# Kernel optimization log

Measured on AMD Instinct MI355X. Metric: run time of the kernel, lower is better.

The kernel has to match this reference:

```python
import jax, jax.numpy as jnp
import numpy as np

D, P, MC = 512, 256, 128   # state dim, obs dim, control dim
H, M, T = 32, 64, 1024     # num filters, Hankel/filter length, horizon
GAMMA = 0.9


def setup_inputs() -> dict:
    rng = np.random.default_rng(0)
    # Stable dynamics: scale spectral radius to 0.95
    A = rng.standard_normal((D, D)).astype(np.float32)
    A *= np.float32(0.95 / np.max(np.abs(np.linalg.eigvals(A))))
    B = (rng.standard_normal((D, MC)) / np.sqrt(D)).astype(np.float32)
    C = (rng.standard_normal((P, D)) / np.sqrt(D)).astype(np.float32)
    # SPD cost matrices
    Q_obs = np.eye(P, dtype=np.float32)
    R = (0.1 * np.eye(MC)).astype(np.float32)
    # LQR-like feedback gain (small, applied to y_obs as in the source)
    K = (0.02 * rng.standard_normal((MC, P))).astype(np.float32)
    # Spectral filters from Hankel matrix: Z_ij = gamma^(i+j+2) * 2/((i+j+2)^3-(i+j+2))
    idx = np.arange(M)
    ij = idx[:, None] + idx[None, :] + 2
    Z = (GAMMA ** ij) * 2.0 / (ij ** 3 - ij)
    w, V = np.linalg.eigh(Z)
    sigma = np.abs(w[-H:])
    phi = V[:, -H:]
    sigma_phi = (sigma ** 0.25)[:, None] * phi.T        # [H, M]
    sigma_phi_M = sigma_phi.astype(np.float32)
    # sum over the inner l-loop of sigma_phi_m (the source sums contributions over l)
    s_m = sigma_phi.sum(axis=1).astype(np.float32)       # [H]
    # Learned controller tensor M_il -> [m_control, H, h, p]
    M_tensor = (0.01 * rng.standard_normal((MC, H, H, P))).astype(np.float32)
    x0 = rng.standard_normal(D).astype(np.float32)
    return {
        "A": jnp.asarray(A), "B": jnp.asarray(B), "C": jnp.asarray(C),
        "Q_obs": jnp.asarray(Q_obs), "R": jnp.asarray(R), "K": jnp.asarray(K),
        "M_tensor": jnp.asarray(M_tensor),
        "sigma_phi_M": jnp.asarray(sigma_phi_M), "s_m": jnp.asarray(s_m),
        "x0": jnp.asarray(x0),
    }


def reference(A, B, C, Q_obs, R, K, M_tensor, sigma_phi_M, s_m, x0):
    h, m = sigma_phi_M.shape          # filters, history window
    mc = B.shape[1]
    p = C.shape[0]

    # CAB[i] = C @ A^i @ B for i = 0..h  (Markov parameters for y_nat)
    def pow_step(Ap, _):
        return Ap @ A, C @ (Ap @ B)
    _, CAB = jax.lax.scan(pow_step, jnp.eye(A.shape[0], dtype=A.dtype), None, length=h + 1)  # [h+1, p, mc]

    # Pre-contract M_tensor with the inner filter weights (sum over j/l):
    # u_pert[c] = sum_{i,k,p'} M2[c,i,p'] * sigma_phi_M[i,k] * y_nat_{t-k}[p']
    M2 = jnp.einsum('cijq,j->ciq', M_tensor, s_m)  # [mc, h, p]

    def step(carry, _):
        x, u_buf, y_buf = carry            # x:[d], u_buf:[h+1,mc] newest-first, y_buf:[m,p] newest-first
        y_obs = C @ x                      # [p]
        # natural observation: strip effect of past controls
        y_nat = y_obs - jnp.einsum('ipc,ic->p', CAB, u_buf)
        y_buf = jnp.concatenate([y_nat[None, :], y_buf[:-1]], axis=0)
        # spectral projection of y_nat history, then contract with learned tensor
        y_proj = sigma_phi_M @ y_buf       # [h, p]
        u_pert = jnp.einsum('ciq,iq->c', M2, y_proj)  # [mc]
        u = -(K @ y_obs) + u_pert
        cost = y_obs @ (Q_obs @ y_obs) + u @ (R @ u)
        u_buf = jnp.concatenate([u[None, :], u_buf[:-1]], axis=0)
        x = A @ x + B @ u
        return (x, u_buf, y_buf), cost

    init = (x0,
            jnp.zeros((h + 1, mc), dtype=x0.dtype),
            jnp.zeros((m, p), dtype=x0.dtype))
    _, costs = jax.lax.scan(step, init, None, length=T)
    return costs  # [T] per-step losses
```

## Files before the change

kernel.cpp:

```cpp
#include <hip/hip_runtime.h>

#define TPB 256
#define MAXJ 48

#define SC_N 128
#define YD0 128
#define YU0 144
#define WD0 151
#define WU0 159
#define DT0 166
#define XP0 182
#define XR0 214
#define U0 230
#define NWG 238
#define NGRP 8
#define GCH 30

__device__ __forceinline__ void cst(float* p, float v) {
  __hip_atomic_store(p, v, __ATOMIC_RELAXED, __HIP_MEMORY_SCOPE_AGENT);
}
__device__ __forceinline__ void cstu(unsigned* p, unsigned v) {
  __hip_atomic_store(p, v, __ATOMIC_RELAXED, __HIP_MEMORY_SCOPE_AGENT);
}
__device__ __forceinline__ unsigned cldu(const unsigned* p) {
  return __hip_atomic_load(p, __ATOMIC_RELAXED, __HIP_MEMORY_SCOPE_AGENT);
}
__device__ __forceinline__ float cld(const float* p) {
  return __hip_atomic_load(p, __ATOMIC_RELAXED, __HIP_MEMORY_SCOPE_AGENT);
}
__device__ __forceinline__ float2 cld2(const float* p) {
  unsigned long long u = __hip_atomic_load(
      reinterpret_cast<const unsigned long long*>(p), __ATOMIC_RELAXED,
      __HIP_MEMORY_SCOPE_AGENT);
  float2 v;
  __builtin_memcpy(&v, &u, 8);
  return v;
}

__device__ __forceinline__ void grid_barrier(unsigned* __restrict__ arr,
                                             unsigned* __restrict__ grp,
                                             int bid, int tid, unsigned phase) {
  asm volatile("s_waitcnt vmcnt(0)" ::: "memory");
  __syncthreads();
  if (tid == 0) cstu(arr + (bid << 5), phase);
  if (bid < NGRP) {
    const int lo = bid * GCH;
    const int n = (NWG - lo < GCH) ? (NWG - lo) : GCH;
    if (tid < n) {
      while (cldu(arr + ((lo + tid) << 5)) < phase) __builtin_amdgcn_s_sleep(1);
    }
    __syncthreads();
    if (tid == 0) cstu(grp + (bid << 5), phase);
  }
  if (tid < NGRP) {
    while (cldu(grp + (tid << 5)) < phase) __builtin_amdgcn_s_sleep(1);
  }
  __atomic_signal_fence(__ATOMIC_SEQ_CST);
  __syncthreads();
}

__device__ void gemm_tile(const float* __restrict__ X, const float* __restrict__ Y,
                          float* __restrict__ Z, int M, int N, int Kd,
                          int mtile, int ntile) {
  __shared__ float Xs[16][65];
  __shared__ float Ys[16][65];
  const int tx = threadIdx.x & 15;
  const int ty = threadIdx.x >> 4;
  const int mbase = mtile * 64;
  const int nbase = ntile * 64;
  float acc[4][4] = {};
  for (int k0 = 0; k0 < Kd; k0 += 16) {
#pragma unroll
    for (int r = 0; r < 4; ++r) {
      int idx = threadIdx.x + 256 * r;
      int mm = idx >> 4, kk = idx & 15;
      int gm = mbase + mm, gk = k0 + kk;
      Xs[kk][mm] = (gm < M && gk < Kd) ? X[(size_t)gm * Kd + gk] : 0.f;
      int nn = idx & 63, k2 = idx >> 6;
      int gn = nbase + nn, gk2 = k0 + k2;
      Ys[k2][nn] = (gk2 < Kd && gn < N) ? Y[(size_t)gk2 * N + gn] : 0.f;
    }
    __syncthreads();
#pragma unroll
    for (int kk = 0; kk < 16; ++kk) {
      float xv[4], yv[4];
#pragma unroll
      for (int a = 0; a < 4; ++a) xv[a] = Xs[kk][ty * 4 + a];
#pragma unroll
      for (int b = 0; b < 4; ++b) yv[b] = Ys[kk][tx * 4 + b];
#pragma unroll
      for (int a = 0; a < 4; ++a)
#pragma unroll
        for (int b = 0; b < 4; ++b) acc[a][b] += xv[a] * yv[b];
    }
    __syncthreads();
  }
#pragma unroll
  for (int a = 0; a < 4; ++a) {
    int gm = mbase + ty * 4 + a;
    if (gm < M) {
#pragma unroll
      for (int b = 0; b < 4; ++b) {
        int gn = nbase + tx * 4 + b;
        if (gn < N) Z[(size_t)gm * N + gn] = acc[a][b];
      }
    }
  }
}

struct JobBatch {
  int n;
  int start[MAXJ + 1];
  int xsel[MAXJ], xoff[MAXJ], ysel[MAXJ], yoff[MAXJ], zoff[MAXJ];
  int M[MAXJ], N[MAXJ], K[MAXJ];
};

__global__ __launch_bounds__(256) void multi_gemm(JobBatch jb,
    const float* __restrict__ A, const float* __restrict__ Bm,
    const float* __restrict__ C, const float* __restrict__ Km,
    float* __restrict__ ws) {
  int b = blockIdx.x;
  int j = 0;
  while (j < jb.n - 1 && b >= jb.start[j + 1]) ++j;
  int rel = b - jb.start[j];
  const float* bases[5] = {ws, A, Bm, C, Km};
  const float* X = bases[jb.xsel[j]] + jb.xoff[j];
  const float* Y = bases[jb.ysel[j]] + jb.yoff[j];
  float* Z = ws + jb.zoff[j];
  int tn = jb.N[j] >> 6;
  gemm_tile(X, Y, Z, jb.M[j], jb.N[j], jb.K[j], rel / tn, rel % tn);
}

__global__ __launch_bounds__(256) void m2_kernel(const float* __restrict__ MT,
    const float* __restrict__ sm, float* __restrict__ M2g) {
  int idx = blockIdx.x * 256 + threadIdx.x;
  if (idx >= 128 * 32 * 256) return;
  int q = idx & 255;
  int ci = idx >> 8;
  const float* base = MT + (size_t)ci * 32 * 256 + q;
  float acc = 0.f;
#pragma unroll
  for (int j = 0; j < 32; ++j) acc += base[j * 256] * sm[j];
  M2g[idx] = acc;
}

__global__ __launch_bounds__(256) void wfir_kernel(const float* __restrict__ M2g,
    const float* __restrict__ Phi, float* __restrict__ W) {
  int idx = blockIdx.x * 256 + threadIdx.x;
  if (idx >= 64 * 32768) return;
  int j = idx >> 15;
  int cq = idx & 32767;
  int c = cq >> 8;
  int q = cq & 255;
  float acc = 0.f;
#pragma unroll
  for (int i = 0; i < 32; ++i)
    acc = fmaf(Phi[(i << 6) | j], M2g[(size_t)(((c << 5) | i) << 8) | q], acc);
  W[idx] = acc;
}

__global__ __launch_bounds__(256) void axpy_acl(const float* __restrict__ A,
    const float* __restrict__ BKC, float* __restrict__ Acl, float* __restrict__ P1) {
  int i = blockIdx.x * 256 + threadIdx.x;
  if (i < 262144) {
    float v = A[i] - BKC[i];
    Acl[i] = v;
    P1[i] = v;
  }
}

__global__ void init_kernel(const float* __restrict__ x0, float* __restrict__ xh,
    float* __restrict__ eh, float* __restrict__ ynh, float* __restrict__ uh0,
    float* __restrict__ dbnd, unsigned* __restrict__ arr,
    unsigned* __restrict__ grp) {
  int i = blockIdx.x * 256 + threadIdx.x;
  int stride = gridDim.x * 256;
  for (int k = i; k < 524288; k += stride) cst(xh + k, 0.f);
  for (int k = i; k < 139264; k += stride) cst(eh + k, 0.f);
  for (int k = i; k < 262144; k += stride) cst(ynh + k, 0.f);
  for (int k = i; k < 8192; k += stride) cst(uh0 + k, 0.f);
  for (int k = i; k < NWG * 32; k += stride) cstu(arr + k, 0u);
  for (int k = i; k < NGRP * 32; k += stride) cstu(grp + k, 0u);
  if (i < 512) cst(dbnd + i, x0[i]);
}

__global__ __launch_bounds__(TPB, 1) void main_kernel(
    const float* __restrict__ B, const float* __restrict__ C,
    const float* __restrict__ x0, const float* __restrict__ Wfir,
    const float* __restrict__ KC, const float* __restrict__ W0C,
    const float* __restrict__ Pp, const float* __restrict__ CAp,
    const float* __restrict__ W0CAp, const float* __restrict__ Rnp,
    const float* __restrict__ AB33p, const float* __restrict__ CAB33p,
    const float* __restrict__ W0CAB33p, const float* __restrict__ A8k,
    float* __restrict__ xh, float* __restrict__ uh0, float* __restrict__ eh,
    float* __restrict__ ynh, float* __restrict__ dbnd,
    unsigned* __restrict__ arr, unsigned* __restrict__ grp) {
  __shared__ float smA[64 * 256];
  __shared__ float smY[8 * 256];
  __shared__ float smV[512];
  __shared__ float smW[8 * 128];
  __shared__ float smVx[8 * 516];
  __shared__ float redsc[4][16];
  const int bid = blockIdx.x;
  const int tid = threadIdx.x;

  if (bid < SC_N) {
    for (int i = tid; i < 16384; i += TPB) {
      int j = i >> 8;
      smA[i] = (j >= 1) ? Wfir[(size_t)j * 32768 + bid * 256 + (i & 255)] : 0.f;
    }
    __syncthreads();
#pragma unroll 1
    for (int ph = 0; ph <= 130; ++ph) {
      if (ph >= 1 && ph < 129) {
        const int Ty = ph * 8 - 8;
        const int c = bid;
        for (int i2 = tid; i2 < 1024; i2 += TPB) {
          float2 v = cld2(ynh + (size_t)Ty * 256 + 2 * i2);
          smY[2 * i2] = v.x;
          smY[2 * i2 + 1] = v.y;
        }
        __syncthreads();
        const int q = tid;
        float yreg[8];
#pragma unroll
        for (int s = 0; s < 8; ++s) yreg[s] = smY[s * 256 + q];
        const int wv = tid >> 6;
        const int lane = tid & 63;
#pragma unroll
        for (int kt = 0; kt < 5; ++kt) {
          const int r0 = 1 + 16 * kt;
          float wreg[23];
#pragma unroll
          for (int i = 0; i < 23; ++i) {
            const int j = r0 - 7 + i;
            wreg[i] = (j >= 1 && j <= 63) ? smA[j * 256 + q] : 0.f;
          }
          float acc[16];
#pragma unroll
          for (int a = 0; a < 16; ++a) acc[a] = 0.f;
#pragma unroll
          for (int a = 0; a < 16; ++a)
#pragma unroll
            for (int s = 0; s < 8; ++s) acc[a] += wreg[a + 7 - s] * yreg[s];
#pragma unroll
          for (int a = 0; a < 16; ++a) {
            float v = acc[a];
            v += __shfl_xor(v, 32);
            v += __shfl_xor(v, 16);
            v += __shfl_xor(v, 8);
            v += __shfl_xor(v, 4);
            v += __shfl_xor(v, 2);
            v += __shfl_xor(v, 1);
            if (lane == 0) redsc[wv][a] = v;
          }
          __syncthreads();
          if (tid < 16) {
            const int r = r0 + tid;
            if (r <= 70) {
              float sum = redsc[0][tid] + redsc[1][tid] + redsc[2][tid] + redsc[3][tid];
              atomicAdd(&eh[(size_t)(Ty + r) * 128 + bid], sum);
            }
          }
          __syncthreads();
        }
        (void)c;
      }
      grid_barrier(arr, grp, bid, tid, (unsigned)(ph + 1));
    }
  } else if (bid < YU0) {
    const int r = bid - YD0;
    const int s = r >> 1;
    const int half = (r & 1) << 7;
    const int row = half + (tid >> 1);
    const int seg = tid & 1;
    const float* Mrow = (s == 0) ? C : (CAp + (size_t)(s - 1) * 131072);
    const float4* m4 = (const float4*)(Mrow + (size_t)row * 512 + seg * 256);
    float4 cm[64];
#pragma unroll
    for (int it = 0; it < 64; ++it) cm[it] = m4[it];
#pragma unroll 1
    for (int ph = 0; ph <= 130; ++ph) {
      if (ph < 128) {
        const int T = ph * 8;
        {
          float2 v = cld2(dbnd + (size_t)ph * 512 + 2 * tid);
          smV[2 * tid] = v.x;
          smV[2 * tid + 1] = v.y;
        }
        __syncthreads();
        const float4* v4 = (const float4*)(smV + seg * 256);
        float a = 0.f;
#pragma unroll
        for (int it = 0; it < 64; ++it) {
          float4 mm = cm[it], vv = v4[it];
          a += mm.x * vv.x + mm.y * vv.y + mm.z * vv.z + mm.w * vv.w;
        }
        a += __shfl_down(a, 1);
        if (seg == 0) atomicAdd(&ynh[(size_t)(T + s) * 256 + row], a);
      }
      grid_barrier(arr, grp, bid, tid, (unsigned)(ph + 1));
    }
  } else if (bid < WD0) {
    const int m = bid - YU0;
    const int row = tid;
    const float4* m4 = (const float4*)(CAB33p + (size_t)m * 32768 + (size_t)row * 128);
    float4 cm[32];
#pragma unroll
    for (int it = 0; it < 32; ++it) cm[it] = m4[it];
#pragma unroll 1
    for (int ph = 0; ph <= 130; ++ph) {
      if (ph < 128) {
        const int T = ph * 8;
        for (int i2 = tid; i2 < 512; i2 += TPB) {
          float2 v = cld2(uh0 + (size_t)(64 + T - 33) * 128 + 2 * i2);
          smW[2 * i2] = v.x;
          smW[2 * i2 + 1] = v.y;
        }
        __syncthreads();
#pragma unroll
        for (int s = 1; s < 8; ++s) {
          if (s > m) {
            const float4* u4 = (const float4*)(smW + (s - m - 1) * 128);
            float a = 0.f;
#pragma unroll
            for (int it = 0; it < 32; ++it) {
              float4 mm = cm[it], vv = u4[it];
              a += mm.x * vv.x + mm.y * vv.y + mm.z * vv.z + mm.w * vv.w;
            }
            atomicAdd(&ynh[(size_t)(T + s) * 256 + row], a);
          }
        }
      }
      grid_barrier(arr, grp, bid, tid, (unsigned)(ph + 1));
    }
  } else if (bid < WU0) {
    const int s = bid - WD0;
    const int row = tid >> 1;
    const int seg = tid & 1;
    const float* Mrow = (s == 0) ? W0C : (W0CAp + (size_t)(s - 1) * 65536);
    const float4* m4 = (const float4*)(Mrow + (size_t)row * 512 + seg * 256);
    float4 cm[64];
#pragma unroll
    for (int it = 0; it < 64; ++it) cm[it] = m4[it];
#pragma unroll 1
    for (int ph = 0; ph <= 130; ++ph) {
      if (ph < 128) {
        const int T = ph * 8;
        {
          float2 v = cld2(dbnd + (size_t)ph * 512 + 2 * tid);
          smV[2 * tid] = v.x;
          smV[2 * tid + 1] = v.y;
        }
        __syncthreads();
        const float4* v4 = (const float4*)(smV + seg * 256);
        float a = 0.f;
#pragma unroll
        for (int it = 0; it < 64; ++it) {
          float4 mm = cm[it], vv = v4[it];
          a += mm.x * vv.x + mm.y * vv.y + mm.z * vv.z + mm.w * vv.w;
        }
        a += __shfl_down(a, 1);
        if (seg == 0) atomicAdd(&eh[(size_t)(T + s) * 128 + row], a);
      }
      grid_barrier(arr, grp, bid, tid, (unsigned)(ph + 1));
    }
  } else if (bid < DT0) {
    const int m = bid - WU0;
    const int row = tid >> 1;
    const int seg = tid & 1;
    const float4* m4 = (const float4*)(W0CAB33p + (size_t)m * 16384 + (size_t)row * 128 + seg * 64);
    float4 cm[16];
#pragma unroll
    for (int it = 0; it < 16; ++it) cm[it] = m4[it];
#pragma unroll 1
    for (int ph = 0; ph <= 130; ++ph) {
      if (ph < 128) {
        const int T = ph * 8;
        for (int i2 = tid; i2 < 512; i2 += TPB) {
          float2 v = cld2(uh0 + (size_t)(64 + T - 33) * 128 + 2 * i2);
          smW[2 * i2] = v.x;
          smW[2 * i2 + 1] = v.y;
        }
        __syncthreads();
#pragma unroll
        for (int s = 1; s < 8; ++s) {
          if (s > m) {
            const float4* u4 = (const float4*)(smW + (s - m - 1) * 128 + seg * 64);
            float a = 0.f;
#pragma unroll
            for (int it = 0; it < 16; ++it) {
              float4 mm = cm[it], vv = u4[it];
              a += mm.x * vv.x + mm.y * vv.y + mm.z * vv.z + mm.w * vv.w;
            }
            a += __shfl_down(a, 1);
            if (seg == 0) atomicAdd(&eh[(size_t)(T + s) * 128 + row], a);
          }
        }
      }
      grid_barrier(arr, grp, bid, tid, (unsigned)(ph + 1));
    }
  } else if (bid < XP0) {
    const int g = bid - DT0;
    const int row = g * 32 + (tid >> 3);
    const int l8 = tid & 7;
    float4 ca[16], cb[32];
    {
      const float4* m4 = (const float4*)(A8k + (size_t)row * 512);
#pragma unroll
      for (int it = 0; it < 16; ++it) ca[it] = m4[it * 8 + l8];
    }
#pragma unroll
    for (int m = 0; m < 8; ++m) {
      const float4* m4 = (const float4*)(AB33p + (size_t)m * 65536 + (size_t)row * 128);
#pragma unroll
      for (int it = 0; it < 4; ++it) cb[m * 4 + it] = m4[it * 8 + l8];
    }
#pragma unroll 1
    for (int ph = 0; ph <= 130; ++ph) {
      if (ph < 127) {
        const int T = ph * 8;
        {
          float2 v = cld2(dbnd + (size_t)ph * 512 + 2 * tid);
          smV[2 * tid] = v.x;
          smV[2 * tid + 1] = v.y;
        }
        for (int i2 = tid; i2 < 512; i2 += TPB) {
          float2 v = cld2(uh0 + (size_t)(64 + T - 33) * 128 + 2 * i2);
          smW[2 * i2] = v.x;
          smW[2 * i2 + 1] = v.y;
        }
        __syncthreads();
        const float4* v4 = (const float4*)smV;
        float a = 0.f;
#pragma unroll
        for (int it = 0; it < 16; ++it) {
          float4 mm = ca[it], vv = v4[it * 8 + l8];
          a += mm.x * vv.x + mm.y * vv.y + mm.z * vv.z + mm.w * vv.w;
        }
#pragma unroll
        for (int m = 0; m < 8; ++m) {
          const float4* w4 = (const float4*)(smW + (7 - m) * 128);
#pragma unroll
          for (int it = 0; it < 4; ++it) {
            float4 mm = cb[m * 4 + it], vv = w4[it * 8 + l8];
            a += mm.x * vv.x + mm.y * vv.y + mm.z * vv.z + mm.w * vv.w;
          }
        }
        a += __shfl_down(a, 4);
        a += __shfl_down(a, 2);
        a += __shfl_down(a, 1);
        if (l8 == 0) cst(&dbnd[(size_t)(ph + 1) * 512 + row], a);
      }
      grid_barrier(arr, grp, bid, tid, (unsigned)(ph + 1));
    }
  } else if (bid < XR0) {
    const int r = bid - XP0;
    const int s = r >> 2;
    const int qtr = (r & 3) << 7;
    const int row = qtr + (tid >> 1);
    const int seg = tid & 1;
    const float4* mp = (const float4*)(Pp + (size_t)s * 262144 + (size_t)row * 512 + seg * 256);
    float4 cm[64];
#pragma unroll
    for (int it = 0; it < 64; ++it) cm[it] = mp[it];
#pragma unroll 1
    for (int ph = 0; ph <= 130; ++ph) {
      if (ph >= 2 && ph < 130) {
        const int Tq = ph * 8 - 16;
        {
          const float* src = (ph == 2) ? x0 : (xh + (size_t)(Tq - 1) * 512);
          float2 v = cld2(src + 2 * tid);
          smV[2 * tid] = v.x;
          smV[2 * tid + 1] = v.y;
        }
        __syncthreads();
        if (ph == 2) {
          if (s == 0) {
            if (seg == 0) atomicAdd(&xh[(size_t)Tq * 512 + row], smV[row]);
          } else {
            const float4* m4 = (const float4*)(Pp + (size_t)(s - 1) * 262144 +
                                               (size_t)row * 512 + seg * 256);
            const float4* v4 = (const float4*)(smV + seg * 256);
            float a = 0.f;
#pragma unroll
            for (int it = 0; it < 64; ++it) {
              float4 mm = m4[it], vv = v4[it];
              a += mm.x * vv.x + mm.y * vv.y + mm.z * vv.z + mm.w * vv.w;
            }
            a += __shfl_down(a, 1);
            if (seg == 0) atomicAdd(&xh[(size_t)(Tq + s) * 512 + row], a);
          }
        } else {
          const float4* v4 = (const float4*)(smV + seg * 256);
          float a = 0.f;
#pragma unroll
          for (int it = 0; it < 64; ++it) {
            float4 mm = cm[it], vv = v4[it];
            a += mm.x * vv.x + mm.y * vv.y + mm.z * vv.z + mm.w * vv.w;
          }
          a += __shfl_down(a, 1);
          if (seg == 0) atomicAdd(&xh[(size_t)(Tq + s) * 512 + row], a);
        }
      }
      grid_barrier(arr, grp, bid, tid, (unsigned)(ph + 1));
    }
  } else if (bid < U0) {
    const int r = bid - XR0;
    const int i = r >> 1;
    const int half = (r & 1) << 8;
    const int row = half + tid;
    const float* Rrow = (i == 0) ? (B + (size_t)row * 128)
                                 : (Rnp + (size_t)(i - 1) * 65536 + (size_t)row * 128);
    const float4* m4 = (const float4*)Rrow;
    float4 cm[32];
#pragma unroll
    for (int it = 0; it < 32; ++it) cm[it] = m4[it];
#pragma unroll 1
    for (int ph = 0; ph <= 130; ++ph) {
      if (ph >= 2 && ph < 130) {
        const int Tq = ph * 8 - 16;
        for (int i2 = tid; i2 < 512; i2 += TPB) {
          int idx = 2 * i2;
          float2 v;
          if (ph == 2 && idx < 128) {
            v.x = 0.f;
            v.y = 0.f;
          } else {
            v = cld2(eh + (size_t)(Tq - 1) * 128 + idx);
          }
          smW[idx] = v.x;
          smW[idx + 1] = v.y;
        }
        __syncthreads();
#pragma unroll
        for (int s = 0; s < 8; ++s) {
          if (s >= i) {
            const float4* e4 = (const float4*)(smW + (s - i) * 128);
            float a = 0.f;
#pragma unroll
            for (int it = 0; it < 32; ++it) {
              float4 mm = cm[it], vv = e4[it];
              a += mm.x * vv.x + mm.y * vv.y + mm.z * vv.z + mm.w * vv.w;
            }
            atomicAdd(&xh[(size_t)(Tq + s) * 512 + row], a);
          }
        }
      }
      grid_barrier(arr, grp, bid, tid, (unsigned)(ph + 1));
    }
  } else {
    const int g = bid - U0;
    const int o = tid >> 1;
    const int par = tid & 1;
    const int s = o >> 4;
    const int lr = o & 15;
    const int row = g * 16 + lr;
    const float4* m4 = (const float4*)(KC + (size_t)row * 512 + par * 256);
    float4 cm[64];
#pragma unroll
    for (int it = 0; it < 64; ++it) cm[it] = m4[it];
#pragma unroll 1
    for (int ph = 0; ph <= 130; ++ph) {
      if (ph >= 3) {
        const int Tu = ph * 8 - 24;
        for (int i2 = tid; i2 < 2048; i2 += TPB) {
          int idx = 2 * i2;
          int rr = idx >> 9;
          int cc = idx & 511;
          float2 v = cld2(xh + (size_t)(Tu + rr) * 512 + cc);
          smVx[rr * 516 + cc] = v.x;
          smVx[rr * 516 + cc + 1] = v.y;
        }
        __syncthreads();
        const float4* v4 = (const float4*)(smVx + s * 516 + par * 256);
        float a = 0.f;
#pragma unroll
        for (int it = 0; it < 64; ++it) {
          float4 mm = cm[it], vv = v4[it];
          a += mm.x * vv.x + mm.y * vv.y + mm.z * vv.z + mm.w * vv.w;
        }
        a += __shfl_down(a, 1);
        if (par == 0) {
          float u = cld(&eh[(size_t)(Tu + s) * 128 + row]) - a;
          cst(&uh0[(size_t)(64 + Tu + s) * 128 + row], u);
        }
      }
      grid_barrier(arr, grp, bid, tid, (unsigned)(ph + 1));
    }
  }
}

__global__ __launch_bounds__(256) void cost_kernel(const float* __restrict__ C,
    const float* __restrict__ Q, const float* __restrict__ R,
    const float* __restrict__ xh, const float* __restrict__ uh0,
    float* __restrict__ out) {
  __shared__ float xs[512];
  __shared__ float ys[256];
  __shared__ float us[128];
  __shared__ float redw[4];
  const int t = blockIdx.x;
  const int tid = threadIdx.x;
  {
    float2 v = cld2(xh + (size_t)t * 512 + 2 * tid);
    xs[2 * tid] = v.x;
    xs[2 * tid + 1] = v.y;
  }
  if (tid < 64) {
    float2 v = cld2(uh0 + (size_t)(64 + t) * 128 + 2 * tid);
    us[2 * tid] = v.x;
    us[2 * tid + 1] = v.y;
  }
  __syncthreads();
  {
    const float4* m4 = (const float4*)(C + (size_t)tid * 512);
    const float4* v4 = (const float4*)xs;
    float a = 0.f;
    for (int it = 0; it < 128; ++it) {
      float4 mm = m4[it], vv = v4[it];
      a += mm.x * vv.x + mm.y * vv.y + mm.z * vv.z + mm.w * vv.w;
    }
    ys[tid] = a;
  }
  __syncthreads();
  float acc;
  {
    const float* Qr = Q + (size_t)tid * 256;
    float qy = 0.f;
    for (int k = 0; k < 256; ++k) qy = fmaf(Qr[k], ys[k], qy);
    acc = qy * ys[tid];
  }
  if (tid < 128) {
    const float* Rr = R + (size_t)tid * 128;
    float ru = 0.f;
    for (int k = 0; k < 128; ++k) ru = fmaf(Rr[k], us[k], ru);
    acc += ru * us[tid];
  }
  float v = acc;
  v += __shfl_xor(v, 32);
  v += __shfl_xor(v, 16);
  v += __shfl_xor(v, 8);
  v += __shfl_xor(v, 4);
  v += __shfl_xor(v, 2);
  v += __shfl_xor(v, 1);
  if ((tid & 63) == 0) redw[tid >> 6] = v;
  __syncthreads();
  if (tid == 0) out[t] = redw[0] + redw[1] + redw[2] + redw[3];
}

extern "C" void kernel_launch(void* const* d_in, const int* in_sizes, int n_in,
                              void* d_out, int out_size, void* d_ws, size_t ws_size,
                              hipStream_t stream) {
  (void)in_sizes; (void)n_in; (void)out_size; (void)ws_size;
  const float* A = (const float*)d_in[0];
  const float* B = (const float*)d_in[1];
  const float* C = (const float*)d_in[2];
  const float* Q = (const float*)d_in[3];
  const float* R = (const float*)d_in[4];
  const float* Km = (const float*)d_in[5];
  const float* MT = (const float*)d_in[6];
  const float* Phi = (const float*)d_in[7];
  const float* sm = (const float*)d_in[8];
  const float* x0 = (const float*)d_in[9];

  float* ws = (float*)d_ws;
  const int oWfir = 0;
  const int oKC = 2097152;
  const int oW0C = 2162688;
  const int oAcl = 2228224;
  const int oP = 2490368;
  const int oCA = 4587520;
  const int oW0CA = 5505024;
  const int oRn = 5963776;
  const int oApB = 6422528;
  const int oAB33 = 6946816;
  const int oCAB33 = 7471104;
  const int oW0CAB33 = 7700480;
  const int oA2 = 7815168;
  const int oA4 = 8077312;
  const int oA8 = 8339456;
  const int oA16 = 8601600;
  const int oA32 = 8863744;
  const int oM2 = 9125888;
  const int oBKC = oM2;
  const int oxh = 10174464;
  const int ouh0 = 10698752;
  const int oeh = 10838016;
  const int oynh = 10977280;
  const int odbnd = 11239424;
  const int oarr = 11306496;
  const int ogrp = oarr + NWG * 32;

  float* xh = ws + oxh;
  float* uh0 = ws + ouh0;
  float* eh = ws + oeh;
  float* ynh = ws + oynh;
  float* dbnd = ws + odbnd;
  unsigned* arr = (unsigned*)(ws + oarr);
  unsigned* grp = (unsigned*)(ws + ogrp);

  JobBatch jb;
  jb.n = 0;
  jb.start[0] = 0;
  auto J = [&](int xs_, int xo, int ys_, int yo, int zo, int M, int N, int K) {
    int i = jb.n++;
    jb.xsel[i] = xs_; jb.xoff[i] = xo; jb.ysel[i] = ys_; jb.yoff[i] = yo;
    jb.zoff[i] = zo; jb.M[i] = M; jb.N[i] = N; jb.K[i] = K;
    jb.start[i + 1] = jb.start[i] + (M >> 6) * (N >> 6);
  };
  auto L = [&]() {
    multi_gemm<<<dim3(jb.start[jb.n]), dim3(256), 0, stream>>>(jb, A, B, C, Km, ws);
    jb.n = 0;
    jb.start[0] = 0;
  };

  init_kernel<<<dim3(2048), dim3(256), 0, stream>>>(x0, xh, eh, ynh, uh0, dbnd,
                                                    arr, grp);
  m2_kernel<<<dim3(4096), dim3(256), 0, stream>>>(MT, sm, ws + oM2);
  wfir_kernel<<<dim3(8192), dim3(256), 0, stream>>>(ws + oM2, Phi, ws + oWfir);

  J(4, 0, 3, 0, oKC, 128, 512, 256);
  J(1, 0, 1, 0, oA2, 512, 512, 512);
  J(1, 0, 2, 0, oApB, 512, 128, 512);
  J(3, 0, 1, 0, oCA, 256, 512, 512);
  L();
  J(2, 0, 0, oKC, oBKC, 512, 512, 128);
  J(0, oA2, 0, oA2, oA4, 512, 512, 512);
  J(0, oCA, 1, 0, oCA + 131072, 256, 512, 512);
  J(1, 0, 0, oApB, oApB + 65536, 512, 128, 512);
  J(0, oWfir, 3, 0, oW0C, 128, 512, 256);
  L();
  axpy_acl<<<dim3(1024), dim3(256), 0, stream>>>(A, ws + oBKC, ws + oAcl, ws + oP);
  J(0, oA4, 0, oA4, oA8, 512, 512, 512);
  J(0, oP, 0, oP, oP + 262144, 512, 512, 512);
  J(0, oCA, 0, oA2, oCA + 2 * 131072, 256, 512, 512);
  J(0, oCA + 131072, 0, oA2, oCA + 3 * 131072, 256, 512, 512);
  J(0, oW0C, 1, 0, oW0CA, 128, 512, 512);
  J(0, oW0C, 0, oA2, oW0CA + 65536, 128, 512, 512);
  J(0, oA2, 0, oApB, oApB + 2 * 65536, 512, 128, 512);
  J(0, oA2, 0, oApB + 65536, oApB + 3 * 65536, 512, 128, 512);
  L();
  J(0, oA8, 0, oA8, oA16, 512, 512, 512);
  J(0, oP, 0, oP + 262144, oP + 2 * 262144, 512, 512, 512);
  J(0, oP + 262144, 0, oP + 262144, oP + 3 * 262144, 512, 512, 512);
  for (int i = 1; i <= 3; ++i)
    J(0, oCA + (i - 1) * 131072, 0, oA4, oCA + (i + 3) * 131072, 256, 512, 512);
  for (int i = 1; i <= 2; ++i)
    J(0, oW0CA + (i - 1) * 65536, 0, oA2, oW0CA + (i + 1) * 65536, 128, 512, 512);
  for (int k = 1; k <= 4; ++k)
    J(0, oA4, 0, oApB + (k - 1) * 65536, oApB + (k + 3) * 65536, 512, 128, 512);
  J(0, oP, 2, 0, oRn, 512, 128, 512);
  J(0, oP + 262144, 2, 0, oRn + 65536, 512, 128, 512);
  L();
  J(0, oA16, 0, oA16, oA32, 512, 512, 512);
  for (int i = 1; i <= 4; ++i)
    J(0, oP + (i - 1) * 262144, 0, oP + 3 * 262144, oP + (i + 3) * 262144, 512, 512, 512);
  for (int i = 1; i <= 3; ++i)
    J(0, oW0CA + (i - 1) * 65536, 0, oA4, oW0CA + (i + 3) * 65536, 128, 512, 512);
  J(0, oP + 2 * 262144, 2, 0, oRn + 2 * 65536, 512, 128, 512);
  J(0, oP + 3 * 262144, 2, 0, oRn + 3 * 65536, 512, 128, 512);
  L();
  for (int m = 0; m <= 7; ++m)
    J(0, oA32, 0, oApB + m * 65536, oAB33 + m * 65536, 512, 128, 512);
  for (int i = 5; i <= 7; ++i)
    J(0, oP + (i - 1) * 262144, 2, 0, oRn + (i - 1) * 65536, 512, 128, 512);
  L();
  for (int m = 0; m <= 6; ++m)
    J(3, 0, 0, oAB33 + m * 65536, oCAB33 + m * 32768, 256, 128, 512);
  for (int m = 0; m <= 6; ++m)
    J(0, oW0C, 0, oAB33 + m * 65536, oW0CAB33 + m * 16384, 128, 128, 512);
  L();

  main_kernel<<<dim3(NWG), dim3(TPB), 0, stream>>>(
      B, C, x0, ws + oWfir, ws + oKC, ws + oW0C, ws + oP, ws + oCA,
      ws + oW0CA, ws + oRn, ws + oAB33, ws + oCAB33, ws + oW0CAB33,
      ws + oA8, xh, uh0, eh, ynh, dbnd, arr, grp);

  cost_kernel<<<dim3(1024), dim3(256), 0, stream>>>(C, Q, R, xh, uh0,
                                                    (float*)d_out);
}
```

Before: 3.353 ms.

## Stream matrix rows from global instead of register-caching in persistent blocks

Removes the large per-thread register arrays that cached matrix rows across all phases in the persistent blocks, reading the matrices from global/L2 on every phase instead. The Y-update blocks are split four-way instead of two-way, which adds workgroups and a wider shuffle reduction. Several multi-step loops are restructured to load each matrix float4 once and reuse it across all time steps. The aim is lower register pressure and spill cost in the barrier-synchronised phase loop, paid for with repeated cache traffic each phase and more blocks taking part in every grid barrier.

```diff
diff --git a/kernel.cpp b/kernel.cpp
--- a/kernel.cpp
+++ b/kernel.cpp
@@ -5,16 +5,16 @@
 
 #define SC_N 128
 #define YD0 128
-#define YU0 144
-#define WD0 151
-#define WU0 159
-#define DT0 166
-#define XP0 182
-#define XR0 214
-#define U0 230
-#define NWG 238
+#define YU0 160
+#define WD0 167
+#define WU0 175
+#define DT0 182
+#define XP0 198
+#define XR0 230
+#define U0 246
+#define NWG 254
 #define NGRP 8
-#define GCH 30
+#define GCH 32
 
 __device__ __forceinline__ void cst(float* p, float v) {
   __hip_atomic_store(p, v, __ATOMIC_RELAXED, __HIP_MEMORY_SCOPE_AGENT);
@@ -214,7 +214,6 @@
     for (int ph = 0; ph <= 130; ++ph) {
       if (ph >= 1 && ph < 129) {
         const int Ty = ph * 8 - 8;
-        const int c = bid;
         for (int i2 = tid; i2 < 1024; i2 += TPB) {
           float2 v = cld2(ynh + (size_t)Ty * 256 + 2 * i2);
           smY[2 * i2] = v.x;
@@ -264,21 +263,17 @@
           }
           __syncthreads();
         }
-        (void)c;
       }
       grid_barrier(arr, grp, bid, tid, (unsigned)(ph + 1));
     }
   } else if (bid < YU0) {
     const int r = bid - YD0;
-    const int s = r >> 1;
-    const int half = (r & 1) << 7;
-    const int row = half + (tid >> 1);
-    const int seg = tid & 1;
+    const int s = r >> 2;
+    const int qtr = (r & 3) * 64;
+    const int row = qtr + (tid >> 2);
+    const int ks = (tid & 3) * 128;
     const float* Mrow = (s == 0) ? C : (CAp + (size_t)(s - 1) * 131072);
-    const float4* m4 = (const float4*)(Mrow + (size_t)row * 512 + seg * 256);
-    float4 cm[64];
-#pragma unroll
-    for (int it = 0; it < 64; ++it) cm[it] = m4[it];
+    const float4* m4 = (const float4*)(Mrow + (size_t)row * 512 + ks);
 #pragma unroll 1
     for (int ph = 0; ph <= 130; ++ph) {
       if (ph < 128) {
@@ -289,15 +284,16 @@
           smV[2 * tid + 1] = v.y;
         }
         __syncthreads();
-        const float4* v4 = (const float4*)(smV + seg * 256);
+        const float4* v4 = (const float4*)(smV + ks);
         float a = 0.f;
 #pragma unroll
-        for (int it = 0; it < 64; ++it) {
-          float4 mm = cm[it], vv = v4[it];
+        for (int it = 0; it < 32; ++it) {
+          float4 mm = m4[it], vv = v4[it];
           a += mm.x * vv.x + mm.y * vv.y + mm.z * vv.z + mm.w * vv.w;
         }
+        a += __shfl_down(a, 2);
         a += __shfl_down(a, 1);
-        if (seg == 0) atomicAdd(&ynh[(size_t)(T + s) * 256 + row], a);
+        if ((tid & 3) == 0) atomicAdd(&ynh[(size_t)(T + s) * 256 + row], a);
       }
       grid_barrier(arr, grp, bid, tid, (unsigned)(ph + 1));
     }
@@ -305,9 +301,6 @@
     const int m = bid - YU0;
     const int row = tid;
     const float4* m4 = (const float4*)(CAB33p + (size_t)m * 32768 + (size_t)row * 128);
-    float4 cm[32];
-#pragma unroll
-    for (int it = 0; it < 32; ++it) cm[it] = m4[it];
 #pragma unroll 1
     for (int ph = 0; ph <= 130; ++ph) {
       if (ph < 128) {
@@ -318,19 +311,23 @@
           smW[2 * i2 + 1] = v.y;
         }
         __syncthreads();
-#pragma unroll
-        for (int s = 1; s < 8; ++s) {
-          if (s > m) {
-            const float4* u4 = (const float4*)(smW + (s - m - 1) * 128);
-            float a = 0.f;
-#pragma unroll
-            for (int it = 0; it < 32; ++it) {
-              float4 mm = cm[it], vv = u4[it];
-              a += mm.x * vv.x + mm.y * vv.y + mm.z * vv.z + mm.w * vv.w;
+        float acc[8];
+#pragma unroll
+        for (int s = 0; s < 8; ++s) acc[s] = 0.f;
+#pragma unroll 4
+        for (int it = 0; it < 32; ++it) {
+          float4 mm = m4[it];
+#pragma unroll
+          for (int s = 0; s < 8; ++s) {
+            if (s > m) {
+              float4 vv = ((const float4*)(smW + (s - m - 1) * 128))[it];
+              acc[s] += mm.x * vv.x + mm.y * vv.y + mm.z * vv.z + mm.w * vv.w;
             }
-            atomicAdd(&ynh[(size_t)(T + s) * 256 + row], a);
-          }
-        }
+          }
+        }
+#pragma unroll
+        for (int s = 0; s < 8; ++s)
+          if (s > m) atomicAdd(&ynh[(size_t)(T + s) * 256 + row], acc[s]);
       }
       grid_barrier(arr, grp, bid, tid, (unsigned)(ph + 1));
     }
@@ -340,9 +337,6 @@
     const int seg = tid & 1;
     const float* Mrow = (s == 0) ? W0C : (W0CAp + (size_t)(s - 1) * 65536);
     const float4* m4 = (const float4*)(Mrow + (size_t)row * 512 + seg * 256);
-    float4 cm[64];
-#pragma unroll
-    for (int it = 0; it < 64; ++it) cm[it] = m4[it];
 #pragma unroll 1
     for (int ph = 0; ph <= 130; ++ph) {
       if (ph < 128) {
@@ -357,7 +351,7 @@
         float a = 0.f;
 #pragma unroll
         for (int it = 0; it < 64; ++it) {
-          float4 mm = cm[it], vv = v4[it];
+          float4 mm = m4[it], vv = v4[it];
           a += mm.x * vv.x + mm.y * vv.y + mm.z * vv.z + mm.w * vv.w;
         }
         a += __shfl_down(a, 1);
@@ -370,9 +364,6 @@
     const int row = tid >> 1;
     const int seg = tid & 1;
     const float4* m4 = (const float4*)(W0CAB33p + (size_t)m * 16384 + (size_t)row * 128 + seg * 64);
-    float4 cm[16];
-#pragma unroll
-    for (int it = 0; it < 16; ++it) cm[it] = m4[it];
 #pragma unroll 1
     for (int ph = 0; ph <= 130; ++ph) {
       if (ph < 128) {
@@ -383,18 +374,26 @@
           smW[2 * i2 + 1] = v.y;
         }
         __syncthreads();
-#pragma unroll
-        for (int s = 1; s < 8; ++s) {
+        float acc[8];
+#pragma unroll
+        for (int s = 0; s < 8; ++s) acc[s] = 0.f;
+#pragma unroll 4
+        for (int it = 0; it < 16; ++it) {
+          float4 mm = m4[it];
+#pragma unroll
+          for (int s = 0; s < 8; ++s) {
+            if (s > m) {
+              float4 vv = ((const float4*)(smW + (s - m - 1) * 128 + seg * 64))[it];
+              acc[s] += mm.x * vv.x + mm.y * vv.y + mm.z * vv.z + mm.w * vv.w;
+            }
+          }
+        }
+#pragma unroll
+        for (int s = 0; s < 8; ++s) {
           if (s > m) {
-            const float4* u4 = (const float4*)(smW + (s - m - 1) * 128 + seg * 64);
-            float a = 0.f;
-#pragma unroll
-            for (int it = 0; it < 16; ++it) {
-              float4 mm = cm[it], vv = u4[it];
-              a += mm.x * vv.x + mm.y * vv.y + mm.z * vv.z + mm.w * vv.w;
-            }
-            a += __shfl_down(a, 1);
-            if (seg == 0) atomicAdd(&eh[(size_t)(T + s) * 128 + row], a);
+            float v = acc[s];
+            v += __shfl_down(v, 1);
+            if (seg == 0) atomicAdd(&eh[(size_t)(T + s) * 128 + row], v);
           }
         }
       }
@@ -404,18 +403,6 @@
     const int g = bid - DT0;
     const int row = g * 32 + (tid >> 3);
     const int l8 = tid & 7;
-    float4 ca[16], cb[32];
-    {
-      const float4* m4 = (const float4*)(A8k + (size_t)row * 512);
-#pragma unroll
-      for (int it = 0; it < 16; ++it) ca[it] = m4[it * 8 + l8];
-    }
-#pragma unroll
-    for (int m = 0; m < 8; ++m) {
-      const float4* m4 = (const float4*)(AB33p + (size_t)m * 65536 + (size_t)row * 128);
-#pragma unroll
-      for (int it = 0; it < 4; ++it) cb[m * 4 + it] = m4[it * 8 + l8];
-    }
 #pragma unroll 1
     for (int ph = 0; ph <= 130; ++ph) {
       if (ph < 127) {
@@ -431,19 +418,23 @@
           smW[2 * i2 + 1] = v.y;
         }
         __syncthreads();
-        const float4* v4 = (const float4*)smV;
         float a = 0.f;
-#pragma unroll
-        for (int it = 0; it < 16; ++it) {
-          float4 mm = ca[it], vv = v4[it * 8 + l8];
-          a += mm.x * vv.x + mm.y * vv.y + mm.z * vv.z + mm.w * vv.w;
+        {
+          const float4* m4 = (const float4*)(A8k + (size_t)row * 512 + l8 * 64);
+          const float4* v4 = (const float4*)(smV + l8 * 64);
+#pragma unroll
+          for (int it = 0; it < 16; ++it) {
+            float4 mm = m4[it], vv = v4[it];
+            a += mm.x * vv.x + mm.y * vv.y + mm.z * vv.z + mm.w * vv.w;
+          }
         }
 #pragma unroll
         for (int m = 0; m < 8; ++m) {
-          const float4* w4 = (const float4*)(smW + (7 - m) * 128);
+          const float4* m4 = (const float4*)(AB33p + (size_t)m * 65536 + (size_t)row * 128 + l8 * 16);
+          const float4* v4 = (const float4*)(smW + (7 - m) * 128 + l8 * 16);
 #pragma unroll
           for (int it = 0; it < 4; ++it) {
-            float4 mm = cb[m * 4 + it], vv = w4[it * 8 + l8];
+            float4 mm = m4[it], vv = v4[it];
             a += mm.x * vv.x + mm.y * vv.y + mm.z * vv.z + mm.w * vv.w;
           }
         }
@@ -460,10 +451,6 @@
     const int qtr = (r & 3) << 7;
     const int row = qtr + (tid >> 1);
     const int seg = tid & 1;
-    const float4* mp = (const float4*)(Pp + (size_t)s * 262144 + (size_t)row * 512 + seg * 256);
-    float4 cm[64];
-#pragma unroll
-    for (int it = 0; it < 64; ++it) cm[it] = mp[it];
 #pragma unroll 1
     for (int ph = 0; ph <= 130; ++ph) {
       if (ph >= 2 && ph < 130) {
@@ -475,28 +462,17 @@
           smV[2 * tid + 1] = v.y;
         }
         __syncthreads();
-        if (ph == 2) {
-          if (s == 0) {
-            if (seg == 0) atomicAdd(&xh[(size_t)Tq * 512 + row], smV[row]);
-          } else {
-            const float4* m4 = (const float4*)(Pp + (size_t)(s - 1) * 262144 +
-                                               (size_t)row * 512 + seg * 256);
-            const float4* v4 = (const float4*)(smV + seg * 256);
-            float a = 0.f;
-#pragma unroll
-            for (int it = 0; it < 64; ++it) {
-              float4 mm = m4[it], vv = v4[it];
-              a += mm.x * vv.x + mm.y * vv.y + mm.z * vv.z + mm.w * vv.w;
-            }
-            a += __shfl_down(a, 1);
-            if (seg == 0) atomicAdd(&xh[(size_t)(Tq + s) * 512 + row], a);
-          }
+        const int pslot = (ph == 2) ? s : (s + 1);
+        if (pslot == 0) {
+          if (seg == 0) atomicAdd(&xh[(size_t)Tq * 512 + row], smV[row]);
         } else {
+          const float4* m4 = (const float4*)(Pp + (size_t)(pslot - 1) * 262144 +
+                                             (size_t)row * 512 + seg * 256);
           const float4* v4 = (const float4*)(smV + seg * 256);
           float a = 0.f;
 #pragma unroll
           for (int it = 0; it < 64; ++it) {
-            float4 mm = cm[it], vv = v4[it];
+            float4 mm = m4[it], vv = v4[it];
             a += mm.x * vv.x + mm.y * vv.y + mm.z * vv.z + mm.w * vv.w;
           }
           a += __shfl_down(a, 1);
@@ -513,9 +489,6 @@
     const float* Rrow = (i == 0) ? (B + (size_t)row * 128)
                                  : (Rnp + (size_t)(i - 1) * 65536 + (size_t)row * 128);
     const float4* m4 = (const float4*)Rrow;
-    float4 cm[32];
-#pragma unroll
-    for (int it = 0; it < 32; ++it) cm[it] = m4[it];
 #pragma unroll 1
     for (int ph = 0; ph <= 130; ++ph) {
       if (ph >= 2 && ph < 130) {
@@ -533,19 +506,23 @@
           smW[idx + 1] = v.y;
         }
         __syncthreads();
-#pragma unroll
-        for (int s = 0; s < 8; ++s) {
-          if (s >= i) {
-            const float4* e4 = (const float4*)(smW + (s - i) * 128);
-            float a = 0.f;
-#pragma unroll
-            for (int it = 0; it < 32; ++it) {
-              float4 mm = cm[it], vv = e4[it];
-              a += mm.x * vv.x + mm.y * vv.y + mm.z * vv.z + mm.w * vv.w;
+        float acc[8];
+#pragma unroll
+        for (int s = 0; s < 8; ++s) acc[s] = 0.f;
+#pragma unroll 4
+        for (int it = 0; it < 32; ++it) {
+          float4 mm = m4[it];
+#pragma unroll
+          for (int s = 0; s < 8; ++s) {
+            if (s >= i) {
+              float4 vv = ((const float4*)(smW + (s - i) * 128))[it];
+              acc[s] += mm.x * vv.x + mm.y * vv.y + mm.z * vv.z + mm.w * vv.w;
             }
-            atomicAdd(&xh[(size_t)(Tq + s) * 512 + row], a);
-          }
-        }
+          }
+        }
+#pragma unroll
+        for (int s = 0; s < 8; ++s)
+          if (s >= i) atomicAdd(&xh[(size_t)(Tq + s) * 512 + row], acc[s]);
       }
       grid_barrier(arr, grp, bid, tid, (unsigned)(ph + 1));
     }
@@ -557,9 +534,6 @@
     const int lr = o & 15;
     const int row = g * 16 + lr;
     const float4* m4 = (const float4*)(KC + (size_t)row * 512 + par * 256);
-    float4 cm[64];
-#pragma unroll
-    for (int it = 0; it < 64; ++it) cm[it] = m4[it];
 #pragma unroll 1
     for (int ph = 0; ph <= 130; ++ph) {
       if (ph >= 3) {
@@ -577,7 +551,7 @@
         float a = 0.f;
 #pragma unroll
         for (int it = 0; it < 64; ++it) {
-          float4 mm = cm[it], vv = v4[it];
+          float4 mm = m4[it], vv = v4[it];
           a += mm.x * vv.x + mm.y * vv.y + mm.z * vv.z + mm.w * vv.w;
         }
         a += __shfl_down(a, 1);
```

New measurement: 3.358 ms. No clear change (+0.1%).
